# Performance work log

Measured on AMD Instinct MI355X. Metric: run time of the kernel, lower is better.

## Reference

```python
import jax, jax.numpy as jnp
import numpy as np

DIST = 3.0
COEFF = 10.0
NEG_SLOPE = 0.3  # keras LeakyReLU default


def _probe_points(dist=DIST):
    # fixed 26 probe offsets on a sphere of radius `dist` (from build())
    angles = np.array(
        [[j * 0.125 - 0.125, i * 0.125 + (j - 1) * 0.0625] for j in range(3) for i in range(8)]
        + [[-0.25, 0.0], [0.25, 0.0]],
        dtype=np.float32,
    ) * (2.0 * np.pi)
    a, b = angles[:, 0], angles[:, 1]
    pts = np.stack([np.sin(a), np.cos(a) * np.cos(b), np.cos(a) * np.sin(b)], axis=-1) * dist
    return jnp.asarray(pts, dtype=jnp.float32)  # (26, 3)


def setup_inputs() -> dict:
    key = jax.random.key(0)
    k1, k2, k3 = jax.random.split(key, 3)
    B, n, f = 2, 1024, 3
    m, out_feats, num_convs = 26, 6, 5
    points = jax.random.normal(k1, (B, n, 3 + f), dtype=jnp.float32)
    # per-conv Dense(m*f -> out_feats) weights/bias, stacked over num_convs
    W = jax.random.normal(k2, (num_convs, m * f, out_feats), dtype=jnp.float32) * 0.1
    b = jax.random.normal(k3, (num_convs, out_feats), dtype=jnp.float32) * 0.1
    return {"points": points, "W": W, "b": b}


def reference(points, W, b):
    B, n, df = points.shape
    d = 3
    f = df - d
    probes = _probe_points()              # (m, d)
    m = probes.shape[0]
    coords = points[..., :d]              # (B, n, d) -> centers too (l = n)
    feats = points[..., d:]               # (B, n, f)
    centers = coords
    # probes per center: (B, l, m, d)
    probes_per_center = centers[:, :, None, :] + probes[None, None, :, :]
    # delta: (B, l, m, n, d)
    delta = coords[:, None, None, :, :] - probes_per_center[:, :, :, None, :]
    sq = jnp.sum(delta * delta, axis=-1)  # (B, l, m, n)
    wgt = COEFF / (sq + COEFF)            # inverse-distance weights
    # weighted feature sum: (B, l, m, f), averaged over n
    wf = jnp.einsum('blmn,bnf->blmf', wgt, feats) / n
    x = wf.reshape(B, n, m * f)           # (B, l, m*f)
    # num_convs parallel Dense + LeakyReLU (Dropout is identity at inference)
    h = jnp.einsum('blx,kxo->blko', x, W) + b[None, None, :, :]
    h = jnp.where(h > 0, h, NEG_SLOPE * h)
    convs = h.reshape(B, n, -1)           # (B, n, num_convs*out_feats)
    return jnp.concatenate([centers, convs], axis=-1)  # (B, n, 3 + 30)
```

## Files before the change

kernel.cpp:

```cpp
#include <hip/hip_runtime.h>


#define NPTS   1024
#define COEFF  10.0f
#define NEG    0.3f

__device__ constexpr float PROBE[26][3] = {
  {-2.12132034f,  1.95984445f, -0.81179415f},
  {-2.12132034f,  1.95984445f,  0.81179415f},
  {-2.12132034f,  0.81179415f,  1.95984445f},
  {-2.12132034f, -0.81179415f,  1.95984445f},
  {-2.12132034f, -1.95984445f,  0.81179415f},
  {-2.12132034f, -1.95984445f, -0.81179415f},
  {-2.12132034f, -0.81179415f, -1.95984445f},
  {-2.12132034f,  0.81179415f, -1.95984445f},
  { 0.0f,         3.0f,         0.0f       },
  { 0.0f,         2.12132034f,  2.12132034f},
  { 0.0f,         0.0f,         3.0f       },
  { 0.0f,        -2.12132034f,  2.12132034f},
  { 0.0f,        -3.0f,         0.0f       },
  { 0.0f,        -2.12132034f, -2.12132034f},
  { 0.0f,         0.0f,        -3.0f       },
  { 0.0f,         2.12132034f, -2.12132034f},
  { 2.12132034f,  1.95984445f,  0.81179415f},
  { 2.12132034f,  0.81179415f,  1.95984445f},
  { 2.12132034f, -0.81179415f,  1.95984445f},
  { 2.12132034f, -1.95984445f,  0.81179415f},
  { 2.12132034f, -1.95984445f, -0.81179415f},
  { 2.12132034f, -0.81179415f, -1.95984445f},
  { 2.12132034f,  0.81179415f, -1.95984445f},
  { 2.12132034f,  1.95984445f, -0.81179415f},
  {-3.0f,         0.0f,         0.0f       },
  { 3.0f,         0.0f,         0.0f       },
};

#define DPP_STEP(x, ctrl, rm, bm, bc)                                        \
  x += __int_as_float(__builtin_amdgcn_update_dpp(                           \
      0, __float_as_int(x), ctrl, rm, bm, bc))

__device__ __forceinline__ float wave_sum_to_lane63(float x) {
  DPP_STEP(x, 0x111, 0xf, 0xf, true);
  DPP_STEP(x, 0x112, 0xf, 0xf, true);
  DPP_STEP(x, 0x114, 0xf, 0xe, false);
  DPP_STEP(x, 0x118, 0xf, 0xc, false);
  DPP_STEP(x, 0x142, 0xa, 0xf, false);
  DPP_STEP(x, 0x143, 0xc, 0xf, false);
  return x;
}

template <int OFF>
__device__ __forceinline__ void run_main(const float* __restrict__ batch,
                                         int lane, float cx, float cy, float cz,
                                         float acc[13][3]) {
  for (int it = 0; it < NPTS / 64; ++it) {
    const float* prow = batch + (it * 64 + lane) * 6;
    const float2 q0 = *reinterpret_cast<const float2*>(prow);
    const float2 q1 = *reinterpret_cast<const float2*>(prow + 2);
    const float2 q2 = *reinterpret_cast<const float2*>(prow + 4);
    const float dx = q0.x - cx, dy = q0.y - cy, dz = q1.x - cz;
    const float f0 = q1.y, f1 = q2.x, f2 = q2.y;
    const float base = fmaf(dx, dx, fmaf(dy, dy, fmaf(dz, dz, 19.0f)));
    #pragma unroll
    for (int j = 0; j < 13; ++j) {
      const float t = fmaf(-2.0f * PROBE[OFF + j][0], dx,
                      fmaf(-2.0f * PROBE[OFF + j][1], dy,
                      fmaf(-2.0f * PROBE[OFF + j][2], dz, base)));
      const float w = __builtin_amdgcn_rcpf(t);
      acc[j][0] = fmaf(w, f0, acc[j][0]);
      acc[j][1] = fmaf(w, f1, acc[j][1]);
      acc[j][2] = fmaf(w, f2, acc[j][2]);
    }
  }
}

__global__ __launch_bounds__(256, 4) void crossconv_kernel(
    const float* __restrict__ points,
    const float* __restrict__ W,
    const float* __restrict__ bias,
    float* __restrict__ out)
{
    __shared__ float sx[2][78];

    const int tid    = threadIdx.x;
    const int lane   = tid & 63;
    const int w      = tid >> 6;
    const int cLocal = w >> 1;
    const int half   = w & 1;
    const int G      = blockIdx.x * 2 + cLocal;

    const float* batch = points + (G >> 10) * (NPTS * 6);
    const float* crow  = points + G * 6;
    const float  cx = crow[0], cy = crow[1], cz = crow[2];

    float acc[13][3];
    #pragma unroll
    for (int j = 0; j < 13; ++j) { acc[j][0] = 0.f; acc[j][1] = 0.f; acc[j][2] = 0.f; }

    if (half == 0) run_main<0>(batch, lane, cx, cy, cz, acc);
    else           run_main<13>(batch, lane, cx, cy, cz, acc);

    const float scale = COEFF / (float)NPTS;
    #pragma unroll
    for (int j = 0; j < 13; ++j) {
      #pragma unroll
      for (int ff = 0; ff < 3; ++ff)
        acc[j][ff] = wave_sum_to_lane63(acc[j][ff]) * scale;
    }

    if (lane == 63) {
      #pragma unroll
      for (int j = 0; j < 13; ++j) {
        sx[cLocal][half * 39 + j * 3 + 0] = acc[j][0];
        sx[cLocal][half * 39 + j * 3 + 1] = acc[j][1];
        sx[cLocal][half * 39 + j * 3 + 2] = acc[j][2];
      }
    }
    __syncthreads();

    if (half == 0) {
      float* orow = out + G * 33;
      if (lane < 30) {
        const int k = lane / 6, o = lane % 6;
        const float* Wk = W + k * (78 * 6) + o;
        float h = bias[lane];
        #pragma unroll
        for (int t = 0; t < 78; ++t)
          h = fmaf(sx[cLocal][t], Wk[t * 6], h);
        h = (h > 0.f) ? h : NEG * h;
        orow[3 + lane] = h;
      } else if (lane < 33) {
        orow[lane - 30] = (lane == 30) ? cx : ((lane == 31) ? cy : cz);
      }
    }
}

extern "C" void kernel_launch(void* const* d_in, const int* in_sizes, int n_in,
                              void* d_out, int out_size, void* d_ws, size_t ws_size,
                              hipStream_t stream) {
    const float* points = (const float*)d_in[0];
    const float* W      = (const float*)d_in[1];
    const float* bias   = (const float*)d_in[2];
    float* out          = (float*)d_out;
    crossconv_kernel<<<1024, 256, 0, stream>>>(points, W, bias, out);
}
```

Baseline: 25.12 us.

## Regroup probes to skip zero-coefficient FMAs, vectorize dense layer, replicate grid

Reassigns the 26 probes between the two waves of each center. Half 0 gets the probes that have zero coordinates, and compile-time template recursion drops the FMAs for those zero coefficients. The per-wave reduction then scatters results to each probe's original slot in shared memory. The final dense layer now reads shared memory as float4 and spreads the sum over four independent accumulators. The launch grid is multiplied by REPLICATE=3, with blocks wrapping via blockIdx&1023, so every output is computed and written three times redundantly. That adds about twice the original work in exchange for more resident waves.

```diff
diff --git a/kernel.cpp b/kernel.cpp
--- a/kernel.cpp
+++ b/kernel.cpp
@@ -1,11 +1,12 @@
 #include <hip/hip_runtime.h>
 
 
-#define NPTS   1024
-#define COEFF  10.0f
-#define NEG    0.3f
+#define NPTS      1024
+#define COEFF     10.0f
+#define NEG       0.3f
+#define REPLICATE 3
 
-__device__ constexpr float PROBE[26][3] = {
+constexpr float PROBE[26][3] = {
   {-2.12132034f,  1.95984445f, -0.81179415f},
   {-2.12132034f,  1.95984445f,  0.81179415f},
   {-2.12132034f,  0.81179415f,  1.95984445f},
@@ -34,6 +35,9 @@
   { 3.0f,         0.0f,         0.0f       },
 };
 
+constexpr int H0[14] = {0,1,2,3,4,5,6,7, 8,12,10,14, 24,25};
+constexpr int H1[14] = {16,17,18,19,20,21,22,23, 9,11,13,15, 0,0};
+
 #define DPP_STEP(x, ctrl, rm, bm, bc)                                        \
   x += __int_as_float(__builtin_amdgcn_update_dpp(                           \
       0, __float_as_int(x), ctrl, rm, bm, bc))
@@ -48,10 +52,37 @@
   return x;
 }
 
-template <int OFF>
+template <int HALF, int J>
+struct ProbeStep {
+  static __device__ __forceinline__ void run(float base, float dx, float dy,
+                                             float dz, float f0, float f1,
+                                             float f2, float* acc) {
+    ProbeStep<HALF, J - 1>::run(base, dx, dy, dz, f0, f1, f2, acc);
+    constexpr int   m   = HALF ? H1[J] : H0[J];
+    constexpr float px2 = -2.0f * PROBE[m][0];
+    constexpr float py2 = -2.0f * PROBE[m][1];
+    constexpr float pz2 = -2.0f * PROBE[m][2];
+    float t = base;
+    if constexpr (px2 != 0.0f) t = fmaf(px2, dx, t);
+    if constexpr (py2 != 0.0f) t = fmaf(py2, dy, t);
+    if constexpr (pz2 != 0.0f) t = fmaf(pz2, dz, t);
+    const float w = __builtin_amdgcn_rcpf(t);
+    acc[J * 3 + 0] = fmaf(w, f0, acc[J * 3 + 0]);
+    acc[J * 3 + 1] = fmaf(w, f1, acc[J * 3 + 1]);
+    acc[J * 3 + 2] = fmaf(w, f2, acc[J * 3 + 2]);
+  }
+};
+template <int HALF>
+struct ProbeStep<HALF, -1> {
+  static __device__ __forceinline__ void run(float, float, float, float,
+                                             float, float, float, float*) {}
+};
+
+template <int HALF>
 __device__ __forceinline__ void run_main(const float* __restrict__ batch,
                                          int lane, float cx, float cy, float cz,
-                                         float acc[13][3]) {
+                                         float* acc) {
+  constexpr int NP = HALF ? 12 : 14;
   for (int it = 0; it < NPTS / 64; ++it) {
     const float* prow = batch + (it * 64 + lane) * 6;
     const float2 q0 = *reinterpret_cast<const float2*>(prow);
@@ -60,15 +91,24 @@
     const float dx = q0.x - cx, dy = q0.y - cy, dz = q1.x - cz;
     const float f0 = q1.y, f1 = q2.x, f2 = q2.y;
     const float base = fmaf(dx, dx, fmaf(dy, dy, fmaf(dz, dz, 19.0f)));
+    ProbeStep<HALF, NP - 1>::run(base, dx, dy, dz, f0, f1, f2, acc);
+  }
+}
+
+template <int HALF>
+__device__ __forceinline__ void reduce_store(float* acc, int lane, int cLocal,
+                                             float sx[2][80], float scale) {
+  constexpr int NP = HALF ? 12 : 14;
+  #pragma unroll
+  for (int j = 0; j < NP * 3; ++j)
+    acc[j] = wave_sum_to_lane63(acc[j]) * scale;
+  if (lane == 63) {
     #pragma unroll
-    for (int j = 0; j < 13; ++j) {
-      const float t = fmaf(-2.0f * PROBE[OFF + j][0], dx,
-                      fmaf(-2.0f * PROBE[OFF + j][1], dy,
-                      fmaf(-2.0f * PROBE[OFF + j][2], dz, base)));
-      const float w = __builtin_amdgcn_rcpf(t);
-      acc[j][0] = fmaf(w, f0, acc[j][0]);
-      acc[j][1] = fmaf(w, f1, acc[j][1]);
-      acc[j][2] = fmaf(w, f2, acc[j][2]);
+    for (int j = 0; j < NP; ++j) {
+      const int m = HALF ? H1[j] : H0[j];
+      sx[cLocal][m * 3 + 0] = acc[j * 3 + 0];
+      sx[cLocal][m * 3 + 1] = acc[j * 3 + 1];
+      sx[cLocal][m * 3 + 2] = acc[j * 3 + 2];
     }
   }
 }
@@ -79,42 +119,30 @@
     const float* __restrict__ bias,
     float* __restrict__ out)
 {
-    __shared__ float sx[2][78];
+    __shared__ __align__(16) float sx[2][80];
 
     const int tid    = threadIdx.x;
     const int lane   = tid & 63;
     const int w      = tid >> 6;
     const int cLocal = w >> 1;
     const int half   = w & 1;
-    const int G      = blockIdx.x * 2 + cLocal;
+    const int bid    = blockIdx.x & 1023;
+    const int G      = bid * 2 + cLocal;
 
     const float* batch = points + (G >> 10) * (NPTS * 6);
     const float* crow  = points + G * 6;
     const float  cx = crow[0], cy = crow[1], cz = crow[2];
 
-    float acc[13][3];
+    float acc[42];
     #pragma unroll
-    for (int j = 0; j < 13; ++j) { acc[j][0] = 0.f; acc[j][1] = 0.f; acc[j][2] = 0.f; }
+    for (int j = 0; j < 42; ++j) acc[j] = 0.f;
 
     if (half == 0) run_main<0>(batch, lane, cx, cy, cz, acc);
-    else           run_main<13>(batch, lane, cx, cy, cz, acc);
+    else           run_main<1>(batch, lane, cx, cy, cz, acc);
 
     const float scale = COEFF / (float)NPTS;
-    #pragma unroll
-    for (int j = 0; j < 13; ++j) {
-      #pragma unroll
-      for (int ff = 0; ff < 3; ++ff)
-        acc[j][ff] = wave_sum_to_lane63(acc[j][ff]) * scale;
-    }
-
-    if (lane == 63) {
-      #pragma unroll
-      for (int j = 0; j < 13; ++j) {
-        sx[cLocal][half * 39 + j * 3 + 0] = acc[j][0];
-        sx[cLocal][half * 39 + j * 3 + 1] = acc[j][1];
-        sx[cLocal][half * 39 + j * 3 + 2] = acc[j][2];
-      }
-    }
+    if (half == 0) reduce_store<0>(acc, lane, cLocal, sx, scale);
+    else           reduce_store<1>(acc, lane, cLocal, sx, scale);
     __syncthreads();
 
     if (half == 0) {
@@ -122,10 +150,20 @@
       if (lane < 30) {
         const int k = lane / 6, o = lane % 6;
         const float* Wk = W + k * (78 * 6) + o;
-        float h = bias[lane];
+        float h0 = bias[lane], h1 = 0.f, h2 = 0.f, h3 = 0.f;
+        const float4* sxv = reinterpret_cast<const float4*>(sx[cLocal]);
         #pragma unroll
-        for (int t = 0; t < 78; ++t)
-          h = fmaf(sx[cLocal][t], Wk[t * 6], h);
+        for (int t4 = 0; t4 < 19; ++t4) {
+          const float4 v = sxv[t4];
+          h0 = fmaf(v.x, Wk[(t4 * 4 + 0) * 6], h0);
+          h1 = fmaf(v.y, Wk[(t4 * 4 + 1) * 6], h1);
+          h2 = fmaf(v.z, Wk[(t4 * 4 + 2) * 6], h2);
+          h3 = fmaf(v.w, Wk[(t4 * 4 + 3) * 6], h3);
+        }
+        const float2 vt = *reinterpret_cast<const float2*>(&sx[cLocal][76]);
+        h0 = fmaf(vt.x, Wk[76 * 6], h0);
+        h1 = fmaf(vt.y, Wk[77 * 6], h1);
+        float h = (h0 + h2) + (h1 + h3);
         h = (h > 0.f) ? h : NEG * h;
         orow[3 + lane] = h;
       } else if (lane < 33) {
@@ -141,5 +179,5 @@
     const float* W      = (const float*)d_in[1];
     const float* bias   = (const float*)d_in[2];
     float* out          = (float*)d_out;
-    crossconv_kernel<<<1024, 256, 0, stream>>>(points, W, bias, out);
+    crossconv_kernel<<<1024 * REPLICATE, 256, 0, stream>>>(points, W, bias, out);
 }
```

Result: slower. 55.55 us (+121.1%).

## Pair symmetric probes, share reciprocals, and use packed FMA for accumulation

Applied to the files above, without the earlier changes.

Regroups the 26 probes into symmetric pairs so each distance term comes from shared partial sums via packed v2f FMAs. Reciprocals are computed in batches of 4 (or 2) with one rcp plus multiplies, cutting transcendental throughput. Feature accumulation uses packed FMA, the per-accumulator scale moves into the dense epilogue, and the dense dot product is split into four accumulators fed by float4 LDS reads. The batched reciprocal risks precision loss or overflow when the product of four distance terms grows large.

```diff
diff --git a/kernel.cpp b/kernel.cpp
--- a/kernel.cpp
+++ b/kernel.cpp
@@ -5,34 +5,19 @@
 #define COEFF  10.0f
 #define NEG    0.3f
 
-__device__ constexpr float PROBE[26][3] = {
-  {-2.12132034f,  1.95984445f, -0.81179415f},
-  {-2.12132034f,  1.95984445f,  0.81179415f},
-  {-2.12132034f,  0.81179415f,  1.95984445f},
-  {-2.12132034f, -0.81179415f,  1.95984445f},
-  {-2.12132034f, -1.95984445f,  0.81179415f},
-  {-2.12132034f, -1.95984445f, -0.81179415f},
-  {-2.12132034f, -0.81179415f, -1.95984445f},
-  {-2.12132034f,  0.81179415f, -1.95984445f},
-  { 0.0f,         3.0f,         0.0f       },
-  { 0.0f,         2.12132034f,  2.12132034f},
-  { 0.0f,         0.0f,         3.0f       },
-  { 0.0f,        -2.12132034f,  2.12132034f},
-  { 0.0f,        -3.0f,         0.0f       },
-  { 0.0f,        -2.12132034f, -2.12132034f},
-  { 0.0f,         0.0f,        -3.0f       },
-  { 0.0f,         2.12132034f, -2.12132034f},
-  { 2.12132034f,  1.95984445f,  0.81179415f},
-  { 2.12132034f,  0.81179415f,  1.95984445f},
-  { 2.12132034f, -0.81179415f,  1.95984445f},
-  { 2.12132034f, -1.95984445f,  0.81179415f},
-  { 2.12132034f, -1.95984445f, -0.81179415f},
-  { 2.12132034f, -0.81179415f, -1.95984445f},
-  { 2.12132034f,  0.81179415f, -1.95984445f},
-  { 2.12132034f,  1.95984445f, -0.81179415f},
-  {-3.0f,         0.0f,         0.0f       },
-  { 3.0f,         0.0f,         0.0f       },
-};
+typedef float v2f __attribute__((ext_vector_type(2)));
+
+__device__ __forceinline__ v2f pkfma(v2f a, v2f b, v2f c) {
+#if __has_builtin(__builtin_elementwise_fma)
+  return __builtin_elementwise_fma(a, b, c);
+#else
+  return v2f{fmaf(a.x, b.x, c.x), fmaf(a.y, b.y, c.y)};
+#endif
+}
+__device__ __forceinline__ v2f splat(float s) { return v2f{s, s}; }
+
+constexpr int M0[14] = {0,5, 1,4, 2,3, 7,6, 8,12, 10,14, 24,25};
+constexpr int M1[12] = {16,19, 17,18, 20,23, 21,22, 9,13, 11,15};
 
 #define DPP_STEP(x, ctrl, rm, bm, bc)                                        \
   x += __int_as_float(__builtin_amdgcn_update_dpp(                           \
@@ -48,27 +33,100 @@
   return x;
 }
 
-template <int OFF>
-__device__ __forceinline__ void run_main(const float* __restrict__ batch,
-                                         int lane, float cx, float cy, float cz,
-                                         float acc[13][3]) {
+__device__ __forceinline__ void rcp4pk(v2f tA, v2f tB, v2f& wA, v2f& wB) {
+  const float pA = tA.x * tA.y;
+  const float pB = tB.x * tB.y;
+  const float r  = __builtin_amdgcn_rcpf(pA * pB);
+  const v2f  rp  = v2f{pB, pA} * r;
+  wA = v2f{tA.y, tA.x} * rp.x;
+  wB = v2f{tB.y, tB.x} * rp.y;
+}
+__device__ __forceinline__ v2f rcp2pk(v2f t) {
+  const float r = __builtin_amdgcn_rcpf(t.x * t.y);
+  return v2f{t.y, t.x} * r;
+}
+
+#define CA 4.24264068f
+#define CY 3.91968890f
+#define CZ 1.62358830f
+
+template <int HALF>
+__device__ void run_main(const float* __restrict__ batch, int lane,
+                         float cx, float cy, float cz, v2f* a01, float* a2) {
+  constexpr int NPAIR = HALF ? 6 : 7;
+  #pragma unroll 2
   for (int it = 0; it < NPTS / 64; ++it) {
     const float* prow = batch + (it * 64 + lane) * 6;
     const float2 q0 = *reinterpret_cast<const float2*>(prow);
     const float2 q1 = *reinterpret_cast<const float2*>(prow + 2);
     const float2 q2 = *reinterpret_cast<const float2*>(prow + 4);
     const float dx = q0.x - cx, dy = q0.y - cy, dz = q1.x - cz;
-    const float f0 = q1.y, f1 = q2.x, f2 = q2.y;
+    const v2f   f01 = {q1.y, q2.x};
+    const float f2  = q2.y;
     const float base = fmaf(dx, dx, fmaf(dy, dy, fmaf(dz, dz, 19.0f)));
+
+    v2f tp[7];
+    if constexpr (HALF == 0) {
+      const float rx = fmaf(CA, dx, base);
+      const float sA = fmaf( CZ, dz, rx);
+      const float sB = fmaf(-CZ, dz, rx);
+      const float sC = fmaf(-CY, dz, rx);
+      const float sD = fmaf( CY, dz, rx);
+      tp[0] = pkfma(v2f{-CY,  CY}, splat(dy), splat(sA));
+      tp[1] = pkfma(v2f{-CY,  CY}, splat(dy), splat(sB));
+      tp[2] = pkfma(v2f{-CZ,  CZ}, splat(dy), splat(sC));
+      tp[3] = pkfma(v2f{-CZ,  CZ}, splat(dy), splat(sD));
+      tp[4] = pkfma(v2f{-6.f, 6.f}, splat(dy), splat(base));
+      tp[5] = pkfma(v2f{-6.f, 6.f}, splat(dz), splat(base));
+      tp[6] = pkfma(v2f{ 6.f,-6.f}, splat(dx), splat(base));
+    } else {
+      const float rx = fmaf(-CA, dx, base);
+      const float sA = fmaf(-CZ, dz, rx);
+      const float sB = fmaf(-CY, dz, rx);
+      const float sC = fmaf( CZ, dz, rx);
+      const float sD = fmaf( CY, dz, rx);
+      tp[0] = pkfma(v2f{-CY,  CY}, splat(dy), splat(sA));
+      tp[1] = pkfma(v2f{-CZ,  CZ}, splat(dy), splat(sB));
+      tp[2] = pkfma(v2f{ CY, -CY}, splat(dy), splat(sC));
+      tp[3] = pkfma(v2f{ CZ, -CZ}, splat(dy), splat(sD));
+      const float u = dy + dz, v = dy - dz;
+      tp[4] = pkfma(v2f{-CA,  CA}, splat(u), splat(base));
+      tp[5] = pkfma(v2f{ CA, -CA}, splat(v), splat(base));
+    }
+
+    v2f wp[7];
+    rcp4pk(tp[0], tp[1], wp[0], wp[1]);
+    rcp4pk(tp[2], tp[3], wp[2], wp[3]);
+    rcp4pk(tp[4], tp[5], wp[4], wp[5]);
+    if constexpr (HALF == 0) wp[6] = rcp2pk(tp[6]);
+
     #pragma unroll
-    for (int j = 0; j < 13; ++j) {
-      const float t = fmaf(-2.0f * PROBE[OFF + j][0], dx,
-                      fmaf(-2.0f * PROBE[OFF + j][1], dy,
-                      fmaf(-2.0f * PROBE[OFF + j][2], dz, base)));
-      const float w = __builtin_amdgcn_rcpf(t);
-      acc[j][0] = fmaf(w, f0, acc[j][0]);
-      acc[j][1] = fmaf(w, f1, acc[j][1]);
-      acc[j][2] = fmaf(w, f2, acc[j][2]);
+    for (int p = 0; p < NPAIR; ++p) {
+      a01[2*p]     = pkfma(splat(wp[p].x), f01, a01[2*p]);
+      a01[2*p + 1] = pkfma(splat(wp[p].y), f01, a01[2*p + 1]);
+      a2[2*p]      = fmaf(wp[p].x, f2, a2[2*p]);
+      a2[2*p + 1]  = fmaf(wp[p].y, f2, a2[2*p + 1]);
+    }
+  }
+}
+
+template <int HALF>
+__device__ __forceinline__ void reduce_store(v2f* a01, float* a2, int lane,
+                                             float* sx) {
+  constexpr int NP = HALF ? 12 : 14;
+  #pragma unroll
+  for (int j = 0; j < NP; ++j) {
+    a01[j].x = wave_sum_to_lane63(a01[j].x);
+    a01[j].y = wave_sum_to_lane63(a01[j].y);
+    a2[j]    = wave_sum_to_lane63(a2[j]);
+  }
+  if (lane == 63) {
+    #pragma unroll
+    for (int j = 0; j < NP; ++j) {
+      const int m = HALF ? M1[j] : M0[j];
+      sx[m * 3 + 0] = a01[j].x;
+      sx[m * 3 + 1] = a01[j].y;
+      sx[m * 3 + 2] = a2[j];
     }
   }
 }
@@ -79,7 +137,7 @@
     const float* __restrict__ bias,
     float* __restrict__ out)
 {
-    __shared__ float sx[2][78];
+    __shared__ __align__(16) float sx[2][80];
 
     const int tid    = threadIdx.x;
     const int lane   = tid & 63;
@@ -92,40 +150,39 @@
     const float* crow  = points + G * 6;
     const float  cx = crow[0], cy = crow[1], cz = crow[2];
 
-    float acc[13][3];
+    v2f   a01[14];
+    float a2[14];
     #pragma unroll
-    for (int j = 0; j < 13; ++j) { acc[j][0] = 0.f; acc[j][1] = 0.f; acc[j][2] = 0.f; }
-
-    if (half == 0) run_main<0>(batch, lane, cx, cy, cz, acc);
-    else           run_main<13>(batch, lane, cx, cy, cz, acc);
-
-    const float scale = COEFF / (float)NPTS;
-    #pragma unroll
-    for (int j = 0; j < 13; ++j) {
-      #pragma unroll
-      for (int ff = 0; ff < 3; ++ff)
-        acc[j][ff] = wave_sum_to_lane63(acc[j][ff]) * scale;
-    }
-
-    if (lane == 63) {
-      #pragma unroll
-      for (int j = 0; j < 13; ++j) {
-        sx[cLocal][half * 39 + j * 3 + 0] = acc[j][0];
-        sx[cLocal][half * 39 + j * 3 + 1] = acc[j][1];
-        sx[cLocal][half * 39 + j * 3 + 2] = acc[j][2];
-      }
-    }
+    for (int j = 0; j < 14; ++j) { a01[j] = v2f{0.f, 0.f}; a2[j] = 0.f; }
+
+    if (half == 0) run_main<0>(batch, lane, cx, cy, cz, a01, a2);
+    else           run_main<1>(batch, lane, cx, cy, cz, a01, a2);
+
+    if (half == 0) reduce_store<0>(a01, a2, lane, sx[cLocal]);
+    else           reduce_store<1>(a01, a2, lane, sx[cLocal]);
     __syncthreads();
 
     if (half == 0) {
+      const float scale = COEFF / (float)NPTS;
       float* orow = out + G * 33;
       if (lane < 30) {
         const int k = lane / 6, o = lane % 6;
         const float* Wk = W + k * (78 * 6) + o;
-        float h = bias[lane];
+        float h0 = 0.f, h1 = 0.f, h2 = 0.f, h3 = 0.f;
+        const float4* sxv = reinterpret_cast<const float4*>(sx[cLocal]);
         #pragma unroll
-        for (int t = 0; t < 78; ++t)
-          h = fmaf(sx[cLocal][t], Wk[t * 6], h);
+        for (int t4 = 0; t4 < 19; ++t4) {
+          const float4 v = sxv[t4];
+          h0 = fmaf(v.x, Wk[(t4 * 4 + 0) * 6], h0);
+          h1 = fmaf(v.y, Wk[(t4 * 4 + 1) * 6], h1);
+          h2 = fmaf(v.z, Wk[(t4 * 4 + 2) * 6], h2);
+          h3 = fmaf(v.w, Wk[(t4 * 4 + 3) * 6], h3);
+        }
+        const float2 vt = *reinterpret_cast<const float2*>(&sx[cLocal][76]);
+        h0 = fmaf(vt.x, Wk[76 * 6], h0);
+        h1 = fmaf(vt.y, Wk[77 * 6], h1);
+        const float dot = (h0 + h2) + (h1 + h3);
+        float h = fmaf(dot, scale, bias[lane]);
         h = (h > 0.f) ? h : NEG * h;
         orow[3 + lane] = h;
       } else if (lane < 33) {
```

Result: faster. 23.84 us (-5.1%).
